# Performance work log

Measured on AMD Instinct MI355X. Metric: run time of the kernel, lower is better.

The kernel has to match this reference:

```python
import jax, jax.numpy as jnp
import numpy as np

D_MODEL = 2048
N_HEADS = 16
HEAD_DIM = D_MODEL // N_HEADS
ROPE_BASE = 10000.0


def rope(x):
    # x: [b, h, s, d]; matches the torch module exactly:
    # x1 = even dims, x2 = odd dims; output = concat([x1*cos - x2*sin, x1*sin + x2*cos], -1)
    b, h, s, d = x.shape
    theta = 1.0 / ROPE_BASE ** (jnp.arange(0, d, 2, dtype=jnp.float32) / d)  # [d/2]
    angles = jnp.arange(s, dtype=jnp.float32)[:, None] * theta[None, :]       # [s, d/2]
    cos = jnp.cos(angles)[None, None]  # [1,1,s,d/2]
    sin = jnp.sin(angles)[None, None]
    x1, x2 = x[..., ::2], x[..., 1::2]
    return jnp.concatenate([x1 * cos - x2 * sin, x1 * sin + x2 * cos], axis=-1)


def setup_inputs() -> dict:
    key = jax.random.key(0)
    ks = jax.random.split(key, 5)
    b, s = 2, 2048
    x = jax.random.normal(ks[0], (b, s, D_MODEL), dtype=jnp.float32)
    scale_in = 1.0 / np.sqrt(D_MODEL)
    Wqkv = jax.random.normal(ks[1], (D_MODEL, 3 * D_MODEL), dtype=jnp.float32) * scale_in
    bqkv = jnp.zeros((3 * D_MODEL,), dtype=jnp.float32)
    Wo = jax.random.normal(ks[2], (D_MODEL, D_MODEL), dtype=jnp.float32) * scale_in
    bo = jnp.zeros((D_MODEL,), dtype=jnp.float32)
    return {"x": x, "Wqkv": Wqkv, "bqkv": bqkv, "Wo": Wo, "bo": bo}


def reference(x, Wqkv, bqkv, Wo, bo):
    b, s, d = x.shape
    qkv = x @ Wqkv + bqkv                      # [b, s, 3d]
    q, k, v = jnp.split(qkv, 3, axis=-1)
    def to_heads(t):
        return t.reshape(b, s, N_HEADS, HEAD_DIM).transpose(0, 2, 1, 3)  # [b,h,s,hd]
    q, k, v = to_heads(q), to_heads(k), to_heads(v)
    q = rope(q)
    k = rope(k)
    scores = jnp.einsum('bhqd,bhkd->bhqk', q, k) / jnp.sqrt(jnp.float32(HEAD_DIM))
    attn = jax.nn.softmax(scores, axis=-1)
    out = jnp.einsum('bhqk,bhkd->bhqd', attn, v)
    out = out.transpose(0, 2, 1, 3).reshape(b, s, d)
    return out @ Wo + bo
```

## Files before the change

### kernel.cpp

```cpp
#include <hip/hip_runtime.h>
#include <hip/hip_bf16.h>
#include <cstdint>
#include <type_traits>

#define D_MODEL 2048
#define NH 16
#define HD 128
#define SEQ 2048
#define QKV_LD (3 * D_MODEL)

typedef __attribute__((ext_vector_type(8))) short short8;
typedef __attribute__((ext_vector_type(4))) float f32x4;
typedef __attribute__((ext_vector_type(16))) float f32x16;

__device__ __forceinline__ ushort f2bf(float f) {
    union { float f; uint32_t u; } c; c.f = f;
    uint32_t u = c.u;
    uint32_t r = (u + 0x7FFFu + ((u >> 16) & 1u)) >> 16;
    return (ushort)r;
}
__device__ __forceinline__ float bf2f(ushort b) {
    union { uint32_t u; float f; } c; c.u = ((uint32_t)b) << 16;
    return c.f;
}

__device__ __forceinline__ void load_lds16(const ushort* g, ushort* l) {
    __builtin_amdgcn_global_load_lds(
        (const __attribute__((address_space(1))) void*)g,
        (__attribute__((address_space(3))) void*)l, 16, 0, 0);
}

__global__ void cvt_bf16_kernel(const float* __restrict__ in, ushort* __restrict__ out, int n4) {
    int idx = blockIdx.x * blockDim.x + threadIdx.x;
    if (idx >= n4) return;
    float4 v = ((const float4*)in)[idx];
    ushort4 o;
    o.x = f2bf(v.x); o.y = f2bf(v.y); o.z = f2bf(v.z); o.w = f2bf(v.w);
    ((ushort4*)out)[idx] = o;
}

__global__ void transpose_bf16_kernel(const float* __restrict__ in, ushort* __restrict__ out,
                                      int R, int C) {
    __shared__ float tile[32][33];
    int tx = threadIdx.x, ty = threadIdx.y;
    int c0 = blockIdx.x * 32, r0 = blockIdx.y * 32;
    for (int i = 0; i < 4; ++i) {
        int r = r0 + ty + i * 8;
        tile[ty + i * 8][tx] = in[(size_t)r * C + c0 + tx];
    }
    __syncthreads();
    for (int i = 0; i < 4; ++i) {
        int c = c0 + ty + i * 8;
        out[(size_t)c * R + r0 + tx] = f2bf(tile[tx][ty + i * 8]);
    }
}

template <typename OutT>
__global__ __launch_bounds__(256) void gemm_bt_bias(
    const ushort* __restrict__ A,
    const ushort* __restrict__ Bt,
    const float* __restrict__ bias,
    OutT* __restrict__ C,
    int M, int N, int K)
{
    __shared__ __align__(16) ushort As[128 * 32];
    __shared__ __align__(16) ushort Bs[128 * 32];
    int t = threadIdx.x;
    int m0 = blockIdx.y * 128, n0 = blockIdx.x * 128;
    int wave = t >> 6, lane = t & 63;
    int wm = (wave & 1) * 64, wn = (wave >> 1) * 64;
    int lr = lane & 15, lh = lane >> 4;

    f32x4 acc[4][4];
    for (int i = 0; i < 4; i++)
        for (int j = 0; j < 4; j++)
            acc[i][j] = (f32x4)0.0f;

    int srow = t >> 2;
    int scol = (t & 3) * 8;
    const ushort* Ag = A + (size_t)(m0 + srow) * K + scol;
    const ushort* Bg = Bt + (size_t)(n0 + srow) * K + scol;
    ushort* AsW = As + wave * 512;
    ushort* BsW = Bs + wave * 512;

    for (int k0 = 0; k0 < K; k0 += 32) {
        __syncthreads();
        load_lds16(Ag + k0, AsW);
        load_lds16(Ag + (size_t)64 * K + k0, AsW + 2048);
        load_lds16(Bg + k0, BsW);
        load_lds16(Bg + (size_t)64 * K + k0, BsW + 2048);
        __syncthreads();
        short8 a[4], b[4];
        for (int i = 0; i < 4; i++)
            a[i] = *(const short8*)(As + (wm + i * 16 + lr) * 32 + lh * 8);
        for (int j = 0; j < 4; j++)
            b[j] = *(const short8*)(Bs + (wn + j * 16 + lr) * 32 + lh * 8);
        for (int i = 0; i < 4; i++)
            for (int j = 0; j < 4; j++)
                acc[i][j] = __builtin_amdgcn_mfma_f32_16x16x32_bf16(a[i], b[j], acc[i][j], 0, 0, 0);
    }

    for (int i = 0; i < 4; i++) {
        int row = m0 + wm + i * 16 + lh * 4;
        for (int j = 0; j < 4; j++) {
            int col = n0 + wn + j * 16 + lr;
            float bv = bias[col];
            for (int r = 0; r < 4; r++) {
                float v = acc[i][j][r] + bv;
                if constexpr (std::is_same<OutT, ushort>::value)
                    C[(size_t)(row + r) * N + col] = f2bf(v);
                else
                    C[(size_t)(row + r) * N + col] = v;
            }
        }
    }
}

__global__ void rope_table(float2* __restrict__ tab) {
    int i = blockIdx.x * blockDim.x + threadIdx.x;
    int s = i >> 6, j = i & 63;
    float theta = powf(10000.0f, -(float)j * (1.0f / 64.0f));
    float ang = (float)s * theta;
    float sn, cs;
    sincosf(ang, &sn, &cs);
    tab[i] = make_float2(cs, sn);
}

__global__ void rope_cast_qk(const ushort* __restrict__ qkv,
                             const float2* __restrict__ tab,
                             ushort* __restrict__ Qb, ushort* __restrict__ Kb) {
    int t = threadIdx.x;
    int wv = blockIdx.x * 4 + (t >> 6);
    int j = t & 63;
    int bs = wv >> 5;
    int rem = wv & 31;
    int which = rem >> 4;
    int h = rem & 15;
    int s = bs & 2047;
    int b = bs >> 11;
    size_t src = (size_t)bs * QKV_LD + which * D_MODEL + h * HD;
    uint32_t pr = *(const uint32_t*)(qkv + src + 2 * j);
    float x1 = bf2f((ushort)(pr & 0xffff));
    float x2 = bf2f((ushort)(pr >> 16));
    float2 cspair = tab[(s << 6) + j];
    float cs = cspair.x, sn = cspair.y;
    float sc = which ? 1.0f : 0.08838834764831845f;
    float o1 = (x1 * cs - x2 * sn) * sc;
    float o2 = (x1 * sn + x2 * cs) * sc;
    ushort* dst = which ? Kb : Qb;
    size_t obase = ((size_t)(b * NH + h) * SEQ + s) * HD;
    dst[obase + j] = f2bf(o1);
    dst[obase + 64 + j] = f2bf(o2);
}

__global__ void v_transpose(const ushort* __restrict__ qkv, ushort* __restrict__ Vt) {
    __shared__ ushort tile[32][33];
    int tx = threadIdx.x, ty = threadIdx.y;
    int s0 = blockIdx.x * 32;
    int d0 = blockIdx.y * 32;
    int bh = blockIdx.z;
    int b = bh >> 4, h = bh & 15;
    for (int i = 0; i < 4; ++i) {
        int s = s0 + ty + i * 8;
        tile[ty + i * 8][tx] = qkv[((size_t)(b * SEQ + s)) * QKV_LD + 2 * D_MODEL + h * HD + d0 + tx];
    }
    __syncthreads();
    for (int i = 0; i < 4; ++i) {
        int d = d0 + ty + i * 8;
        Vt[((size_t)bh * HD + d) * SEQ + s0 + tx] = tile[tx][ty + i * 8];
    }
}

__global__ __launch_bounds__(256) void attn_mfma(const ushort* __restrict__ Qb,
                                                 const ushort* __restrict__ Kb,
                                                 const ushort* __restrict__ Vt,
                                                 ushort* __restrict__ ctx) {
    __shared__ ushort smem[25600];
    ushort* Ks = smem;
    ushort* Vts = smem + 8192;
    ushort* Ps = smem + 16384;

    int t = threadIdx.x;
    int w = t >> 6, l = t & 63;
    int l31 = l & 31, g = l >> 5;
    int q0 = blockIdx.x * 128;
    int bh = blockIdx.y;
    int b = bh >> 4, h = bh & 15;

    int qrow = q0 + w * 32 + l31;
    const ushort* Qg = Qb + ((size_t)bh * SEQ + qrow) * HD;
    short8 qf[8];
#pragma unroll
    for (int kc = 0; kc < 8; kc++)
        qf[kc] = *(const short8*)(Qg + kc * 16 + g * 8);

    f32x16 O[4];
#pragma unroll
    for (int di = 0; di < 4; di++) O[di] = (f32x16)0.0f;
    float m_run = -INFINITY, l_run = 0.0f;

    const ushort* KgB = Kb + (size_t)bh * SEQ * HD;
    const ushort* VtB = Vt + (size_t)bh * HD * SEQ;

    for (int k0 = 0; k0 < SEQ; k0 += 64) {
        __syncthreads();
#pragma unroll
        for (int c2 = 0; c2 < 4; c2++) {
            int f = c2 * 256 + t;
            int r = f >> 4, c = f & 15;
            int cp = c ^ (r & 15);
            uint4 v = *(const uint4*)(KgB + (size_t)(k0 + r) * HD + c * 8);
            *(uint4*)(Ks + r * 128 + cp * 8) = v;
        }
#pragma unroll
        for (int c2 = 0; c2 < 4; c2++) {
            int f = c2 * 256 + t;
            int d = f >> 3, c = f & 7;
            int cp = c ^ (d & 7);
            uint4 v = *(const uint4*)(VtB + (size_t)d * SEQ + k0 + c * 8);
            *(uint4*)(Vts + d * 64 + cp * 8) = v;
        }
        __syncthreads();

        f32x16 St[2];
        St[0] = (f32x16)0.0f;
        St[1] = (f32x16)0.0f;
#pragma unroll
        for (int ki = 0; ki < 2; ki++) {
            int row = ki * 32 + l31;
#pragma unroll
            for (int kc = 0; kc < 8; kc++) {
                int cp = (kc * 2 + g) ^ (row & 15);
                short8 a = *(const short8*)(Ks + row * 128 + cp * 8);
                St[ki] = __builtin_amdgcn_mfma_f32_32x32x16_bf16(a, qf[kc], St[ki], 0, 0, 0);
            }
        }

        float mx = -INFINITY;
#pragma unroll
        for (int ki = 0; ki < 2; ki++)
#pragma unroll
            for (int r = 0; r < 16; r++) mx = fmaxf(mx, St[ki][r]);
        mx = fmaxf(mx, __shfl_xor(mx, 32));
        float mn = fmaxf(m_run, mx);
        float alpha = __expf(m_run - mn);
        m_run = mn;
        float psum = 0.0f;
#pragma unroll
        for (int ki = 0; ki < 2; ki++)
#pragma unroll
            for (int r = 0; r < 16; r++) {
                float p = __expf(St[ki][r] - mn);
                St[ki][r] = p;
                psum += p;
            }
        psum += __shfl_xor(psum, 32);
        l_run = l_run * alpha + psum;
#pragma unroll
        for (int di = 0; di < 4; di++)
#pragma unroll
            for (int r = 0; r < 16; r++) O[di][r] *= alpha;

        {
            int qloc = w * 32 + l31;
            ushort* Pr = Ps + qloc * 72;
#pragma unroll
            for (int ki = 0; ki < 2; ki++)
#pragma unroll
                for (int u = 0; u < 4; u++) {
                    ushort4 pk;
                    pk.x = f2bf(St[ki][4 * u + 0]);
                    pk.y = f2bf(St[ki][4 * u + 1]);
                    pk.z = f2bf(St[ki][4 * u + 2]);
                    pk.w = f2bf(St[ki][4 * u + 3]);
                    *(ushort4*)(Pr + ki * 32 + 8 * u + 4 * g) = pk;
                }
        }

        {
            int qloc = w * 32 + l31;
            short8 pb[4];
#pragma unroll
            for (int kc = 0; kc < 4; kc++)
                pb[kc] = *(const short8*)(Ps + qloc * 72 + kc * 16 + g * 8);
#pragma unroll
            for (int di = 0; di < 4; di++) {
                int d = di * 32 + l31;
#pragma unroll
                for (int kc = 0; kc < 4; kc++) {
                    int cp = (kc * 2 + g) ^ (d & 7);
                    short8 va = *(const short8*)(Vts + d * 64 + cp * 8);
                    O[di] = __builtin_amdgcn_mfma_f32_32x32x16_bf16(va, pb[kc], O[di], 0, 0, 0);
                }
            }
        }
    }

    __syncthreads();
    float inv = 1.0f / l_run;
    ushort* ob = smem;
    {
        int qloc = w * 32 + l31;
        ushort* orow = ob + qloc * 128;
#pragma unroll
        for (int di = 0; di < 4; di++)
#pragma unroll
            for (int u = 0; u < 4; u++) {
                ushort4 pk;
                pk.x = f2bf(O[di][4 * u + 0] * inv);
                pk.y = f2bf(O[di][4 * u + 1] * inv);
                pk.z = f2bf(O[di][4 * u + 2] * inv);
                pk.w = f2bf(O[di][4 * u + 3] * inv);
                *(ushort4*)(orow + di * 32 + 8 * u + 4 * g) = pk;
            }
    }
#pragma unroll
    for (int p = 0; p < 8; p++) {
        int qloc = w * 32 + p * 4 + (l >> 4);
        int c16 = l & 15;
        uint4 v = *(const uint4*)(ob + qloc * 128 + c16 * 8);
        size_t tok = (size_t)b * SEQ + q0 + qloc;
        *(uint4*)(ctx + tok * D_MODEL + h * HD + c16 * 8) = v;
    }
}

extern "C" void kernel_launch(void* const* d_in, const int* in_sizes, int n_in,
                              void* d_out, int out_size, void* d_ws, size_t ws_size,
                              hipStream_t stream) {
    const float* x    = (const float*)d_in[0];
    const float* Wqkv = (const float*)d_in[1];
    const float* bqkv = (const float*)d_in[2];
    const float* Wo   = (const float*)d_in[3];
    const float* bo   = (const float*)d_in[4];
    float* out = (float*)d_out;

    char* ws = (char*)d_ws;
    ushort* x_bf   = (ushort*)(ws);
    ushort* wqkvT  = (ushort*)(ws + 16777216);
    ushort* woT    = (ushort*)(ws + 41943040);
    ushort* qkv_bf = (ushort*)(ws + 50331648);
    ushort* Qb     = (ushort*)(ws + 100663296);
    ushort* Kb     = (ushort*)(ws + 117440512);
    ushort* VtG    = (ushort*)(ws + 134217728);
    ushort* ctx    = (ushort*)(ws + 150994944);
    float2* rtab   = (float2*)(ws + 150994944);

    rope_table<<<512, 256, 0, stream>>>(rtab);
    cvt_bf16_kernel<<<8192, 256, 0, stream>>>(x, x_bf, 2097152);
    transpose_bf16_kernel<<<dim3(192, 64), dim3(32, 8), 0, stream>>>(Wqkv, wqkvT, 2048, 6144);
    transpose_bf16_kernel<<<dim3(64, 64), dim3(32, 8), 0, stream>>>(Wo, woT, 2048, 2048);
    gemm_bt_bias<ushort><<<dim3(48, 32), 256, 0, stream>>>(x_bf, wqkvT, bqkv, qkv_bf, 4096, 6144, 2048);
    rope_cast_qk<<<32768, 256, 0, stream>>>(qkv_bf, rtab, Qb, Kb);
    v_transpose<<<dim3(64, 4, 32), dim3(32, 8), 0, stream>>>(qkv_bf, VtG);
    attn_mfma<<<dim3(16, 32), 256, 0, stream>>>(Qb, Kb, VtG, ctx);
    gemm_bt_bias<float><<<dim3(16, 32), 256, 0, stream>>>(ctx, woT, bo, out, 4096, 2048, 2048);
}
```

Baseline: 468.7 us.

## Replace GEMM with 256x256 tile, double-buffered, swizzled-LDS pipelined kernel

Replaces the 128x128 single-buffered GEMM with a 256x256-tile, 512-thread kernel. It uses BK=64, double-buffered LDS with an XOR swizzle against bank conflicts, and interleaves global-to-LDS staging with MFMA phases under barriers and setprio. The aim is more data reuse per tile and hidden load latency for the QKV and output projections. In exchange it needs 128KB of LDS per block, and the output projection launches only 128 blocks, which may underfill the CUs.

```diff
diff --git a/kernel.cpp b/kernel.cpp
--- a/kernel.cpp
+++ b/kernel.cpp
@@ -55,58 +55,114 @@
     }
 }
 
+#define STAGE_A(L, T_, B_) load_lds16(Ag + (size_t)(L) * 64 * K + (size_t)(T_) * 64, \
+                                      smA + (B_) * 16384 + (L) * 4096 + ldsW)
+#define STAGE_B(L, T_, B_) load_lds16(Bg + (size_t)(L) * 64 * K + (size_t)(T_) * 64, \
+                                      smB + (B_) * 16384 + (L) * 4096 + ldsW)
+#define READ_A(MH) do { const ushort* _ab = smA + cb * 16384 + aRow + (MH) * 4096; \
+    _Pragma("unroll") for (int i_ = 0; i_ < 4; ++i_) { \
+        af[i_][0] = *(const short8*)(_ab + i_ * 1024 + pc0); \
+        af[i_][1] = *(const short8*)(_ab + i_ * 1024 + pc1); } } while (0)
+#define READ_B(NHh) do { const ushort* _bb = smB + cb * 16384 + bRow + (NHh) * 2048; \
+    _Pragma("unroll") for (int j_ = 0; j_ < 2; ++j_) { \
+        bfr[j_][0] = *(const short8*)(_bb + j_ * 1024 + pc0); \
+        bfr[j_][1] = *(const short8*)(_bb + j_ * 1024 + pc1); } } while (0)
+#define MFMA16(MH, NHh) do { \
+    _Pragma("unroll") for (int i_ = 0; i_ < 4; ++i_) \
+    _Pragma("unroll") for (int j_ = 0; j_ < 2; ++j_) { \
+        acc[(MH) * 4 + i_][(NHh) * 2 + j_] = __builtin_amdgcn_mfma_f32_16x16x32_bf16( \
+            af[i_][0], bfr[j_][0], acc[(MH) * 4 + i_][(NHh) * 2 + j_], 0, 0, 0); \
+        acc[(MH) * 4 + i_][(NHh) * 2 + j_] = __builtin_amdgcn_mfma_f32_16x16x32_bf16( \
+            af[i_][1], bfr[j_][1], acc[(MH) * 4 + i_][(NHh) * 2 + j_], 0, 0, 0); } } while (0)
+
 template <typename OutT>
-__global__ __launch_bounds__(256) void gemm_bt_bias(
+__global__ __launch_bounds__(512, 2) void gemm256(
     const ushort* __restrict__ A,
     const ushort* __restrict__ Bt,
     const float* __restrict__ bias,
     OutT* __restrict__ C,
     int M, int N, int K)
 {
-    __shared__ __align__(16) ushort As[128 * 32];
-    __shared__ __align__(16) ushort Bs[128 * 32];
+    __shared__ __align__(16) ushort sm[65536];
+    ushort* smA = sm;
+    ushort* smB = sm + 32768;
+
     int t = threadIdx.x;
-    int m0 = blockIdx.y * 128, n0 = blockIdx.x * 128;
-    int wave = t >> 6, lane = t & 63;
-    int wm = (wave & 1) * 64, wn = (wave >> 1) * 64;
+    int w = t >> 6, lane = t & 63;
     int lr = lane & 15, lh = lane >> 4;
-
-    f32x4 acc[4][4];
-    for (int i = 0; i < 4; i++)
-        for (int j = 0; j < 4; j++)
-            acc[i][j] = (f32x4)0.0f;
-
-    int srow = t >> 2;
-    int scol = (t & 3) * 8;
+    int wm_idx = w >> 2, wn_idx = w & 3;
+    int m0 = blockIdx.y * 256, n0 = blockIdx.x * 256;
+
+    int srow = t >> 3;
+    int scol = ((t & 7) ^ (srow & 7)) << 3;
     const ushort* Ag = A + (size_t)(m0 + srow) * K + scol;
     const ushort* Bg = Bt + (size_t)(n0 + srow) * K + scol;
-    ushort* AsW = As + wave * 512;
-    ushort* BsW = Bs + wave * 512;
-
-    for (int k0 = 0; k0 < K; k0 += 32) {
-        __syncthreads();
-        load_lds16(Ag + k0, AsW);
-        load_lds16(Ag + (size_t)64 * K + k0, AsW + 2048);
-        load_lds16(Bg + k0, BsW);
-        load_lds16(Bg + (size_t)64 * K + k0, BsW + 2048);
-        __syncthreads();
-        short8 a[4], b[4];
-        for (int i = 0; i < 4; i++)
-            a[i] = *(const short8*)(As + (wm + i * 16 + lr) * 32 + lh * 8);
-        for (int j = 0; j < 4; j++)
-            b[j] = *(const short8*)(Bs + (wn + j * 16 + lr) * 32 + lh * 8);
-        for (int i = 0; i < 4; i++)
-            for (int j = 0; j < 4; j++)
-                acc[i][j] = __builtin_amdgcn_mfma_f32_16x16x32_bf16(a[i], b[j], acc[i][j], 0, 0, 0);
-    }
-
-    for (int i = 0; i < 4; i++) {
-        int row = m0 + wm + i * 16 + lh * 4;
-        for (int j = 0; j < 4; j++) {
-            int col = n0 + wn + j * 16 + lr;
-            float bv = bias[col];
-            for (int r = 0; r < 4; r++) {
-                float v = acc[i][j][r] + bv;
+    int ldsW = w * 512;
+
+    int pc0 = (lh ^ (lr & 7)) << 3;
+    int pc1 = ((4 + lh) ^ (lr & 7)) << 3;
+    int aRow = (wm_idx * 128 + lr) * 64;
+    int bRow = (wn_idx * 64 + lr) * 64;
+
+    f32x4 acc[8][4];
+#pragma unroll
+    for (int i = 0; i < 8; ++i)
+#pragma unroll
+        for (int j = 0; j < 4; ++j) acc[i][j] = (f32x4)0.0f;
+    short8 af[4][2], bfr[2][2];
+
+    int NT = K >> 6;
+
+    STAGE_A(0, 0, 0); STAGE_A(1, 0, 0); STAGE_A(2, 0, 0); STAGE_A(3, 0, 0);
+    STAGE_B(0, 0, 0); STAGE_B(1, 0, 0); STAGE_B(2, 0, 0); STAGE_B(3, 0, 0);
+    if (NT > 1) {
+        STAGE_A(0, 1, 1); STAGE_A(2, 1, 1);
+        asm volatile("s_waitcnt vmcnt(2)" ::: "memory");
+    } else {
+        asm volatile("s_waitcnt vmcnt(0)" ::: "memory");
+    }
+    __builtin_amdgcn_s_barrier();
+    __builtin_amdgcn_sched_barrier(0);
+
+    for (int T = 0; T < NT; ++T) {
+        int cb = T & 1, nb = cb ^ 1;
+        READ_A(0); READ_B(0);
+        if (T + 1 < NT) { STAGE_A(1, T + 1, nb); STAGE_A(3, T + 1, nb); }
+        __builtin_amdgcn_s_barrier();
+        __builtin_amdgcn_s_setprio(1); MFMA16(0, 0); __builtin_amdgcn_s_setprio(0);
+        __builtin_amdgcn_s_barrier();
+        READ_B(1);
+        if (T + 1 < NT) { STAGE_B(0, T + 1, nb); STAGE_B(1, T + 1, nb); }
+        __builtin_amdgcn_s_barrier();
+        __builtin_amdgcn_s_setprio(1); MFMA16(0, 1); __builtin_amdgcn_s_setprio(0);
+        __builtin_amdgcn_s_barrier();
+        READ_A(1); READ_B(0);
+        if (T + 1 < NT) { STAGE_B(2, T + 1, nb); STAGE_B(3, T + 1, nb); }
+        if (T + 2 < NT) { STAGE_A(0, T + 2, cb); STAGE_A(2, T + 2, cb); }
+        __builtin_amdgcn_s_barrier();
+        __builtin_amdgcn_s_setprio(1); MFMA16(1, 0); __builtin_amdgcn_s_setprio(0);
+        __builtin_amdgcn_s_barrier();
+        READ_B(1);
+        __builtin_amdgcn_s_barrier();
+        __builtin_amdgcn_s_setprio(1); MFMA16(1, 1); __builtin_amdgcn_s_setprio(0);
+        if (T + 2 < NT) asm volatile("s_waitcnt vmcnt(2)" ::: "memory");
+        else            asm volatile("s_waitcnt vmcnt(0)" ::: "memory");
+        __builtin_amdgcn_s_barrier();
+        __builtin_amdgcn_sched_barrier(0);
+    }
+
+    float bv[4];
+#pragma unroll
+    for (int jj = 0; jj < 4; ++jj) bv[jj] = bias[n0 + wn_idx * 64 + jj * 16 + lr];
+#pragma unroll
+    for (int ii = 0; ii < 8; ++ii) {
+        int row = m0 + wm_idx * 128 + ii * 16 + lh * 4;
+#pragma unroll
+        for (int jj = 0; jj < 4; ++jj) {
+            int col = n0 + wn_idx * 64 + jj * 16 + lr;
+#pragma unroll
+            for (int r = 0; r < 4; ++r) {
+                float v = acc[ii][jj][r] + bv[jj];
                 if constexpr (std::is_same<OutT, ushort>::value)
                     C[(size_t)(row + r) * N + col] = f2bf(v);
                 else
@@ -349,9 +405,9 @@
     cvt_bf16_kernel<<<8192, 256, 0, stream>>>(x, x_bf, 2097152);
     transpose_bf16_kernel<<<dim3(192, 64), dim3(32, 8), 0, stream>>>(Wqkv, wqkvT, 2048, 6144);
     transpose_bf16_kernel<<<dim3(64, 64), dim3(32, 8), 0, stream>>>(Wo, woT, 2048, 2048);
-    gemm_bt_bias<ushort><<<dim3(48, 32), 256, 0, stream>>>(x_bf, wqkvT, bqkv, qkv_bf, 4096, 6144, 2048);
+    gemm256<ushort><<<dim3(24, 16), 512, 0, stream>>>(x_bf, wqkvT, bqkv, qkv_bf, 4096, 6144, 2048);
     rope_cast_qk<<<32768, 256, 0, stream>>>(qkv_bf, rtab, Qb, Kb);
     v_transpose<<<dim3(64, 4, 32), dim3(32, 8), 0, stream>>>(qkv_bf, VtG);
     attn_mfma<<<dim3(16, 32), 256, 0, stream>>>(Qb, Kb, VtG, ctx);
-    gemm_bt_bias<float><<<dim3(16, 32), 256, 0, stream>>>(ctx, woT, bo, out, 4096, 2048, 2048);
-}
+    gemm256<float><<<dim3(8, 16), 512, 0, stream>>>(ctx, woT, bo, out, 4096, 2048, 2048);
+}
```

New measurement: 450.5 us. 3.9% less time.
